# Performance work log

Measured on AMD Instinct MI355X. Metric: run time of the kernel, lower is better.

The kernel has to match this reference:

```python
import jax, jax.numpy as jnp
import numpy as np

T = 8
TAU = 2.0       # spikingjelly LIFNode default tau
VTH = 1.0       # default v_threshold
ALPHA = 2.0     # surrogate.ATan alpha
EPS = 1e-5      # BatchNorm eps


@jax.custom_vjp
def spike_fn(x):
    # Heaviside with ATan surrogate gradient
    return (x >= 0.0).astype(x.dtype)

def _spike_fwd(x):
    return (x >= 0.0).astype(x.dtype), x

def _spike_bwd(x, g):
    sg = (ALPHA / 2.0) / (1.0 + (jnp.pi / 2.0 * ALPHA * x) ** 2)
    return (g * sg,)

spike_fn.defvjp(_spike_fwd, _spike_bwd)


def lif(x_seq):
    """Multi-step LIF over leading time axis. decay_input=True, hard reset to 0, detach_reset."""
    def step(v, x):
        v = v + (x - v) / TAU            # charge
        s = spike_fn(v - VTH)            # fire (surrogate grad)
        v = v * (1.0 - jax.lax.stop_gradient(s))  # detached hard reset to v_reset=0
        return v, s
    _, s_seq = jax.lax.scan(step, jnp.zeros_like(x_seq[0]), x_seq)
    return s_seq


def conv2d(x, w, b, stride):
    y = jax.lax.conv_general_dilated(x, w, (stride, stride), 'VALID',
                                     dimension_numbers=('NCHW', 'OIHW', 'NCHW'))
    return y + b[None, :, None, None]


def batchnorm(x, g, b):
    # training-mode BN over merged (T*B, H, W) axes, matching step_mode='m' BatchNorm2d
    m = x.mean((0, 2, 3), keepdims=True)
    v = x.var((0, 2, 3), keepdims=True)
    return g[None, :, None, None] * (x - m) * jax.lax.rsqrt(v + EPS) + b[None, :, None, None]


def setup_inputs() -> dict:
    key = jax.random.key(0)
    ks = jax.random.split(key, 12)
    def w_init(k, shape):
        fan_in = int(np.prod(shape[1:]))
        return jax.random.normal(k, shape, dtype=jnp.float32) / np.sqrt(fan_in)
    x = jax.random.normal(ks[0], (128, 4, 84, 84), dtype=jnp.float32)
    return {
        'x': x,
        'conv1_w': w_init(ks[1], (32, 4, 8, 8)),  'conv1_b': jnp.zeros((32,), jnp.float32),
        'bn1_g': jnp.ones((32,), jnp.float32),    'bn1_b': jnp.zeros((32,), jnp.float32),
        'conv2_w': w_init(ks[2], (64, 32, 4, 4)), 'conv2_b': jnp.zeros((64,), jnp.float32),
        'bn2_g': jnp.ones((64,), jnp.float32),    'bn2_b': jnp.zeros((64,), jnp.float32),
        'conv3_w': w_init(ks[3], (64, 64, 3, 3)), 'conv3_b': jnp.zeros((64,), jnp.float32),
        'bn3_g': jnp.ones((64,), jnp.float32),    'bn3_b': jnp.zeros((64,), jnp.float32),
        'fc1_w': w_init(ks[4], (512, 3136)),      'fc1_b': jnp.zeros((512,), jnp.float32),
        'fco_w': w_init(ks[5], (2, 512)),         'fco_b': jnp.zeros((2,), jnp.float32),
    }


def reference(x, conv1_w, conv1_b, bn1_g, bn1_b, conv2_w, conv2_b, bn2_g, bn2_b,
              conv3_w, conv3_b, bn3_g, bn3_b, fc1_w, fc1_b, fco_w, fco_b):
    B = x.shape[0]
    # replicate input over T timesteps; fold T into batch for conv/BN (step_mode='m')
    xs = jnp.broadcast_to(x, (T,) + x.shape).reshape((T * B,) + x.shape[1:])

    h = batchnorm(conv2d(xs, conv1_w, conv1_b, 4), bn1_g, bn1_b)   # [TB,32,20,20]
    s = lif(h.reshape((T, B) + h.shape[1:]))
    h = s.reshape((T * B,) + s.shape[2:])

    h = batchnorm(conv2d(h, conv2_w, conv2_b, 2), bn2_g, bn2_b)    # [TB,64,9,9]
    s = lif(h.reshape((T, B) + h.shape[1:]))
    h = s.reshape((T * B,) + s.shape[2:])

    h = batchnorm(conv2d(h, conv3_w, conv3_b, 1), bn3_g, bn3_b)    # [TB,64,7,7]
    s = lif(h.reshape((T, B) + h.shape[1:]))                        # [T,B,64,7,7]

    feat = s.reshape(T, B, -1)                                      # [T,B,3136]
    hid = lif(jnp.einsum('tbi,oi->tbo', feat, fc1_w) + fc1_b)       # [T,B,512]
    out_seq = jnp.einsum('tbo,ko->tbk', hid, fco_w) + fco_b         # [T,B,2]
    return out_seq.mean(0)                                          # [B,2]
```

## Files before the change

### kernel.cpp

```cpp
#include <hip/hip_runtime.h>
#include <cstdint>
#include <cstddef>

#define TT 8

#define H1_ELEMS (128*32*20*20)
#define E2_ELEMS (128*64*81)
#define E3_ELEMS (128*64*49)

typedef __attribute__((ext_vector_type(8))) short short8;
typedef __attribute__((ext_vector_type(4))) float f32x4;

__global__ void prep_wT1(const float* __restrict__ w1, float* __restrict__ wT1) {
  int i = blockIdx.x * 256 + threadIdx.x;
  if (i >= 8192) return;
  int oc = i >> 8, pos = i & 255;
  wT1[(oc >> 4) * 4096 + pos * 16 + (oc & 15)] = w1[oc * 256 + pos];
}

__global__ void prep_w2frag(const float* __restrict__ w2, __bf16* __restrict__ wf) {
  int i = blockIdx.x * 256 + threadIdx.x;
  if (i >= 98304) return;
  int j    = i & 7;
  int oc   = (i >> 3) & 63;
  int quad = (i >> 9) & 3;
  int ksg  = (i >> 11) & 15;
  int term = i >> 15;
  int k = ksg * 32 + quad * 8 + j;
  int ci = k >> 4, kpos = k & 15;
  float w = w2[oc * 512 + ci * 16 + kpos];
  float hf = (float)(__bf16)w;
  float r1 = w - hf;
  float mf = (float)(__bf16)r1;
  float r2 = r1 - mf;
  __bf16 val = (term == 0) ? (__bf16)w : (term == 1) ? (__bf16)r1 : (__bf16)r2;
  wf[i] = val;
}

__global__ void prep_w3frag(const float* __restrict__ w3, __bf16* __restrict__ wf) {
  int i = blockIdx.x * 256 + threadIdx.x;
  if (i >= 110592) return;
  int j    = i & 7;
  int oc   = (i >> 3) & 63;
  int quad = (i >> 9) & 3;
  int tk   = i >> 11;
  int term = tk / 18, kstep = tk % 18;
  int k = kstep * 32 + quad * 8 + j;
  int pos = k >> 6, ci = k & 63;
  float w = w3[oc * 576 + ci * 9 + pos];
  float hf = (float)(__bf16)w;
  float r1 = w - hf;
  float mf = (float)(__bf16)r1;
  float r2 = r1 - mf;
  __bf16 val = (term == 0) ? (__bf16)w : (term == 1) ? (__bf16)r1 : (__bf16)r2;
  wf[i] = val;
}

__global__ void prep_wff(const float* __restrict__ w, __bf16* __restrict__ wf) {
  int i = blockIdx.x * 256 + threadIdx.x;
  if (i >= 602112) return;
  int oc   = i & 511;
  int quad = (i >> 9) & 3;
  int ts   = i >> 11;
  int term = ts / 98, s = ts - term * 98;
  int kbase = s * 32 + quad * 8;
  int pos = kbase >> 6;
  int ci0 = kbase & 63;
  union { __bf16 h[8]; short8 v; } V;
  #pragma unroll
  for (int j = 0; j < 8; j++) {
    float wv = w[(size_t)oc * 3136 + (ci0 + j) * 49 + pos];
    float hf = (float)(__bf16)wv;
    float r1 = wv - hf;
    float mf = (float)(__bf16)r1;
    float r2 = r1 - mf;
    V.h[j] = (term == 0) ? (__bf16)wv : (term == 1) ? (__bf16)r1 : (__bf16)r2;
  }
  *(short8*)(wf + (size_t)i * 8) = V.v;
}

__global__ __launch_bounds__(128) void k_conv1(const float* __restrict__ x,
                                               const float* __restrict__ wT,
                                               const float* __restrict__ bias,
                                               float* __restrict__ out) {
  __shared__ float xt[8064];
  int tid = threadIdx.x;
  int img = blockIdx.x >> 2;
  int q   = blockIdx.x & 3;
  int och = blockIdx.y;
  float4* dst = (float4*)xt;
  #pragma unroll
  for (int ci = 0; ci < 4; ci++) {
    const float4* s4 = (const float4*)(x + (size_t)img * 28224 + ci * 7056 + q * 1680);
    for (int i = tid; i < 504; i += 128) dst[ci * 504 + i] = s4[i];
  }
  __syncthreads();
  if (tid >= 100) return;
  int oyl = tid / 20, ox = tid % 20;
  float acc[16];
  #pragma unroll
  for (int j = 0; j < 16; j++) acc[j] = 0.f;
  int xb0 = oyl * 336 + ox * 4;
  const float* wh = wT + och * 4096;
  #pragma unroll 1
  for (int ci = 0; ci < 4; ci++) {
    #pragma unroll 1
    for (int ky = 0; ky < 8; ky++) {
      const float* xr = xt + ci * 2016 + xb0 + ky * 84;
      float4 xa  = *(const float4*)xr;
      float4 xbv = *(const float4*)(xr + 4);
      const float* wr = wh + (ci * 8 + ky) * 128;
      float xs[8] = {xa.x, xa.y, xa.z, xa.w, xbv.x, xbv.y, xbv.z, xbv.w};
      #pragma unroll
      for (int kx = 0; kx < 8; kx++) {
        #pragma unroll
        for (int j = 0; j < 16; j++)
          acc[j] = fmaf(xs[kx], wr[kx * 16 + j], acc[j]);
      }
    }
  }
  size_t obase = (size_t)img * 12800 + och * 6400 + (q * 5 + oyl) * 20 + ox;
  #pragma unroll
  for (int j = 0; j < 16; j++) out[obase + j * 400] = acc[j] + bias[och * 16 + j];
}

template <int HW>
__global__ void k_bnpartial(const float* __restrict__ xp, int C, int Nper,
                            float* __restrict__ pout) {
  int c = blockIdx.x, s = blockIdx.y, S = gridDim.y, tid = threadIdx.x;
  int n = Nper * HW;
  float sum = 0.f, sum2 = 0.f;
  for (int i = tid; i < n; i += 256) {
    int nb = s * Nper + i / HW;
    int p  = i % HW;
    float v = xp[((size_t)nb * C + c) * HW + p];
    sum += v; sum2 += v * v;
  }
  __shared__ float l0[256], l1[256];
  l0[tid] = sum; l1[tid] = sum2; __syncthreads();
  for (int k = 128; k > 0; k >>= 1) {
    if (tid < k) { l0[tid] += l0[tid + k]; l1[tid] += l1[tid + k]; }
    __syncthreads();
  }
  if (tid == 0) { pout[(c * S + s) * 2] = l0[0]; pout[(c * S + s) * 2 + 1] = l1[0]; }
}

__global__ void k_bnfinal(const float* __restrict__ pin, int S, float n,
                          float* __restrict__ meanArr, float* __restrict__ rstdArr) {
  int c = blockIdx.x, lane = threadIdx.x;
  float s = 0.f, s2 = 0.f;
  if (lane < S) { s = pin[(c * S + lane) * 2]; s2 = pin[(c * S + lane) * 2 + 1]; }
  for (int off = 8; off > 0; off >>= 1) { s += __shfl_down(s, off); s2 += __shfl_down(s2, off); }
  if (lane == 0) {
    float m = s / n;
    float var = s2 / n - m * m;
    meanArr[c] = m;
    rstdArr[c] = rsqrtf(var + 1e-5f);
  }
}

__global__ void k_lif1b(const float* __restrict__ h, const float* __restrict__ mean,
                        const float* __restrict__ rstd, const float* __restrict__ g,
                        const float* __restrict__ bb, uint32_t* __restrict__ sout) {
  int idx = blockIdx.x * 256 + threadIdx.x;
  int ic = idx / 20;
  int ci = ic & 31;
  const float* hp = h + (size_t)idx * 20;
  float gm = g[ci], mm = mean[ci], rs = rstd[ci], bc = bb[ci];
  float xv[20];
  #pragma unroll
  for (int j4 = 0; j4 < 5; j4++) {
    float4 hv = ((const float4*)hp)[j4];
    xv[j4 * 4 + 0] = gm * (hv.x - mm) * rs + bc;
    xv[j4 * 4 + 1] = gm * (hv.y - mm) * rs + bc;
    xv[j4 * 4 + 2] = gm * (hv.z - mm) * rs + bc;
    xv[j4 * 4 + 3] = gm * (hv.w - mm) * rs + bc;
  }
  float v[20];
  #pragma unroll
  for (int j = 0; j < 20; j++) v[j] = 0.f;
  #pragma unroll
  for (int t = 0; t < TT; t++) {
    uint32_t w = 0;
    #pragma unroll
    for (int j = 0; j < 20; j++) {
      v[j] = v[j] + (xv[j] - v[j]) * 0.5f;
      uint32_t s = (v[j] >= 1.0f);
      w |= s << j;
      if (s) v[j] = 0.f;
    }
    sout[t * 81920 + idx] = w;
  }
}

template <int W, int NROW>
__global__ void k_lifb(const float* __restrict__ h, const float* __restrict__ mean,
                       const float* __restrict__ rstd, const float* __restrict__ g,
                       const float* __restrict__ bb, uint32_t* __restrict__ sout,
                       int E) {
  int idx = blockIdx.x * 256 + threadIdx.x;
  int bc = idx / NROW;
  int c = bc & 63;
  float gm = g[c], mm = mean[c], rs = rstd[c], bcn = bb[c];
  float v[W];
  #pragma unroll
  for (int j = 0; j < W; j++) v[j] = 0.f;
  int nword = 128 * 64 * NROW;
  #pragma unroll
  for (int t = 0; t < TT; t++) {
    const float* hp = h + (size_t)t * E + (size_t)idx * W;
    uint32_t w = 0;
    #pragma unroll
    for (int j = 0; j < W; j++) {
      float xv = gm * (hp[j] - mm) * rs + bcn;
      v[j] = v[j] + (xv - v[j]) * 0.5f;
      uint32_t s = (v[j] >= 1.0f);
      w |= s << j;
      if (s) v[j] = 0.f;
    }
    sout[t * nword + idx] = w;
  }
}

__global__ __launch_bounds__(256) void k_conv2m(const uint32_t* __restrict__ s1b,
                                                const __bf16* __restrict__ wf,
                                                const float* __restrict__ bias,
                                                float* __restrict__ out) {
  __shared__ uint32_t sp[1280];
  __shared__ uint4 wl4[3072];
  __bf16* wl = (__bf16*)wl4;
  int tid = threadIdx.x;
  int img0 = blockIdx.x * 2;
  {
    const uint32_t* src = s1b + (size_t)img0 * 640;
    for (int i = tid; i < 1280; i += 256) sp[i] = src[i];
  }
  int wave = tid >> 6, lane = tid & 63;
  int img_local = wave >> 1;
  int tg = wave & 1;
  int l15 = lane & 15, quad = lane >> 4;
  int ci_off = quad >> 1;
  int kyp = (quad & 1) * 2;
  int spb[3], sh[3];
  #pragma unroll
  for (int mt = 0; mt < 3; mt++) {
    int px = tg * 48 + mt * 16 + l15;
    if (px > 80) px = 80;
    int oy = px / 9, ox = px - oy * 9;
    sh[mt]  = ox * 2;
    spb[mt] = img_local * 640 + ci_off * 20 + oy * 2 + kyp;
  }
  f32x4 acc[3][4];
  #pragma unroll
  for (int mt = 0; mt < 3; mt++)
    #pragma unroll
    for (int nt = 0; nt < 4; nt++) acc[mt][nt] = (f32x4){0.f, 0.f, 0.f, 0.f};

  for (int kc = 0; kc < 4; kc++) {
    __syncthreads();
    for (int o = tid * 8; o < 24576; o += 2048) {
      int tk = o >> 11;
      int term = tk >> 2, ksl = tk & 3;
      const __bf16* src = wf + (((term * 16 + kc * 4 + ksl)) << 11) + (o & 2047);
      *(uint4*)(wl + o) = *(const uint4*)src;
    }
    __syncthreads();
    #pragma unroll
    for (int ks = 0; ks < 4; ks++) {
      int ksg = kc * 4 + ks;
      short8 a[3];
      #pragma unroll
      for (int mt = 0; mt < 3; mt++) {
        uint32_t w0 = sp[spb[mt] + ksg * 40];
        uint32_t w1 = sp[spb[mt] + ksg * 40 + 1];
        uint32_t n0 = (w0 >> sh[mt]) & 15u;
        uint32_t n1 = (w1 >> sh[mt]) & 15u;
        union { uint32_t u[4]; short8 v; } A;
        A.u[0] = ((n0 & 1u) ? 0x3F80u : 0u) | ((n0 & 2u) ? 0x3F800000u : 0u);
        A.u[1] = ((n0 & 4u) ? 0x3F80u : 0u) | ((n0 & 8u) ? 0x3F800000u : 0u);
        A.u[2] = ((n1 & 1u) ? 0x3F80u : 0u) | ((n1 & 2u) ? 0x3F800000u : 0u);
        A.u[3] = ((n1 & 4u) ? 0x3F80u : 0u) | ((n1 & 8u) ? 0x3F800000u : 0u);
        a[mt] = A.v;
      }
      #pragma unroll
      for (int term = 0; term < 3; term++) {
        int fb = ((term * 4 + ks) << 11) + (quad << 9);
        #pragma unroll
        for (int nt = 0; nt < 4; nt++) {
          short8 b = *(const short8*)(wl + fb + ((nt << 4) + l15) * 8);
          #pragma unroll
          for (int mt = 0; mt < 3; mt++)
            acc[mt][nt] = __builtin_amdgcn_mfma_f32_16x16x32_bf16(a[mt], b, acc[mt][nt], 0, 0, 0);
        }
      }
    }
  }
  #pragma unroll
  for (int nt = 0; nt < 4; nt++) {
    int oc = nt * 16 + l15;
    float bv = bias[oc];
    float* op = out + ((size_t)(img0 + img_local) * 64 + oc) * 81;
    #pragma unroll
    for (int mt = 0; mt < 3; mt++) {
      int pxr = tg * 48 + mt * 16 + quad * 4;
      #pragma unroll
      for (int r = 0; r < 4; r++) {
        int px = pxr + r;
        if (px < 81) op[px] = acc[mt][nt][r] + bv;
      }
    }
  }
}

__global__ void k_s2T(const uint32_t* __restrict__ sbits, uint32_t* __restrict__ s2T) {
  __shared__ uint32_t sb[576];
  int n = blockIdx.x;
  int t = n >> 7, b = n & 127;
  int tid = threadIdx.x;
  const uint32_t* src = sbits + t * 73728 + b * 576;
  for (int i = tid; i < 576; i += 256) sb[i] = src[i];
  __syncthreads();
  if (tid >= 162) return;
  int half = tid & 1, pc = tid >> 1;
  int r = pc / 9, cpix = pc - r * 9;
  uint32_t w = 0;
  #pragma unroll
  for (int ci = 0; ci < 32; ci++)
    w |= (((sb[(half * 32 + ci) * 9 + r] >> cpix) & 1u) << ci);
  s2T[(size_t)n * 162 + pc * 2 + half] = w;
}

__global__ __launch_bounds__(256) void k_conv3m(const uint32_t* __restrict__ s2T,
                                                const __bf16* __restrict__ wf,
                                                const float* __restrict__ bias,
                                                float* __restrict__ out) {
  __shared__ uint32_t sp[324];
  __shared__ uint4 wl4[4608];
  __bf16* wl = (__bf16*)wl4;
  int tid = threadIdx.x;
  int img0 = blockIdx.x * 2;
  {
    const uint32_t* src = s2T + (size_t)img0 * 162;
    for (int i = tid; i < 324; i += 256) sp[i] = src[i];
  }
  int wave = tid >> 6, lane = tid & 63;
  int img_local = wave >> 1, tg = wave & 1;
  int l15 = lane & 15, quad = lane >> 4;
  int qsh = quad * 8;
  int base[2];
  #pragma unroll
  for (int mt = 0; mt < 2; mt++) {
    int px = tg * 32 + mt * 16 + l15;
    if (px > 48) px = 48;
    int oy = px / 7, ox = px - oy * 7;
    base[mt] = img_local * 162 + (oy * 9 + ox) * 2;
  }
  f32x4 acc[2][4];
  #pragma unroll
  for (int mt = 0; mt < 2; mt++)
    #pragma unroll
    for (int nt = 0; nt < 4; nt++) acc[mt][nt] = (f32x4){0.f, 0.f, 0.f, 0.f};

  #pragma unroll
  for (int kc = 0; kc < 3; kc++) {
    __syncthreads();
    #pragma unroll
    for (int it = 0; it < 18; it++) {
      const __bf16* s = wf + (((it / 6) * 18 + kc * 6 + (it % 6)) << 11) + tid * 8;
      *(uint4*)(wl + (it << 11) + tid * 8) = *(const uint4*)s;
    }
    __syncthreads();
    #pragma unroll
    for (int ksl = 0; ksl < 6; ksl++) {
      int kstep = kc * 6 + ksl;
      int pos = kstep >> 1, cihalf = kstep & 1;
      int ky = pos / 3, kx = pos % 3;
      short8 a[2];
      #pragma unroll
      for (int mt = 0; mt < 2; mt++) {
        uint32_t word = sp[base[mt] + (ky * 9 + kx) * 2 + cihalf];
        uint32_t byt = (word >> qsh) & 255u;
        union { uint32_t u[4]; short8 v; } A;
        A.u[0] = ((byt & 1u)  ? 0x3F80u : 0u) | ((byt & 2u)   ? 0x3F800000u : 0u);
        A.u[1] = ((byt & 4u)  ? 0x3F80u : 0u) | ((byt & 8u)   ? 0x3F800000u : 0u);
        A.u[2] = ((byt & 16u) ? 0x3F80u : 0u) | ((byt & 32u)  ? 0x3F800000u : 0u);
        A.u[3] = ((byt & 64u) ? 0x3F80u : 0u) | ((byt & 128u) ? 0x3F800000u : 0u);
        a[mt] = A.v;
      }
      #pragma unroll
      for (int term = 0; term < 3; term++) {
        int fb = ((term * 6 + ksl) << 11) + (quad << 9);
        #pragma unroll
        for (int nt = 0; nt < 4; nt++) {
          short8 b = *(const short8*)(wl + fb + ((nt << 4) + l15) * 8);
          #pragma unroll
          for (int mt = 0; mt < 2; mt++)
            acc[mt][nt] = __builtin_amdgcn_mfma_f32_16x16x32_bf16(a[mt], b, acc[mt][nt], 0, 0, 0);
        }
      }
    }
  }
  #pragma unroll
  for (int nt = 0; nt < 4; nt++) {
    int oc = nt * 16 + l15;
    float bv = bias[oc];
    float* op = out + ((size_t)(img0 + img_local) * 64 + oc) * 49;
    #pragma unroll
    for (int mt = 0; mt < 2; mt++) {
      int pxr = tg * 32 + mt * 16 + quad * 4;
      #pragma unroll
      for (int r = 0; r < 4; r++) {
        int px = pxr + r;
        if (px < 49) op[px] = acc[mt][nt][r] + bv;
      }
    }
  }
}

__global__ void k_s3T(const uint32_t* __restrict__ sbits, uint32_t* __restrict__ s3T) {
  __shared__ uint32_t sb[896];
  int r0 = blockIdx.x * 2;
  int tid = threadIdx.x;
  for (int i = tid; i < 896; i += 256) {
    int rl = i / 448, o = i - rl * 448;
    int row = r0 + rl;
    sb[i] = sbits[(row >> 7) * 57344 + (row & 127) * 448 + o];
  }
  __syncthreads();
  if (tid >= 196) return;
  int rl = tid / 98, k = tid - rl * 98;
  int pos = k >> 1, half = k & 1;
  int py = pos / 7, px = pos - py * 7;
  const uint32_t* base = sb + rl * 448 + half * 224 + py;
  uint32_t w = 0;
  #pragma unroll
  for (int ci = 0; ci < 32; ci++)
    w |= ((base[ci * 7] >> px) & 1u) << ci;
  s3T[(size_t)(r0 + rl) * 98 + k] = w;
}

__global__ __launch_bounds__(256) void k_fc1m(const uint32_t* __restrict__ s3T,
                                              const __bf16* __restrict__ wf,
                                              float* __restrict__ part) {
  __shared__ uint32_t aS[6272];
  int tid = threadIdx.x;
  int row0 = blockIdx.x * 64;
  int oc0  = blockIdx.y * 32;
  {
    const uint32_t* src = s3T + (size_t)row0 * 98;
    for (int i = tid; i < 6272; i += 256) aS[i] = src[i];
  }
  __syncthreads();
  int wave = tid >> 6, lane = tid & 63;
  int l15 = lane & 15, quad = lane >> 4;
  int qsh = quad * 8;
  f32x4 acc[4][2];
  #pragma unroll
  for (int mt = 0; mt < 4; mt++)
    #pragma unroll
    for (int nt = 0; nt < 2; nt++) acc[mt][nt] = (f32x4){0.f, 0.f, 0.f, 0.f};
  int nIter = (wave < 2) ? 25 : 24;
  #pragma unroll 1
  for (int i = 0; i < nIter; i++) {
    int ks = i * 4 + wave;
    short8 a[4];
    #pragma unroll
    for (int mt = 0; mt < 4; mt++) {
      uint32_t word = aS[(mt * 16 + l15) * 98 + ks];
      uint32_t byt = (word >> qsh) & 255u;
      union { uint32_t u[4]; short8 v; } A;
      A.u[0] = ((byt & 1u)  ? 0x3F80u : 0u) | ((byt & 2u)   ? 0x3F800000u : 0u);
      A.u[1] = ((byt & 4u)  ? 0x3F80u : 0u) | ((byt & 8u)   ? 0x3F800000u : 0u);
      A.u[2] = ((byt & 16u) ? 0x3F80u : 0u) | ((byt & 32u)  ? 0x3F800000u : 0u);
      A.u[3] = ((byt & 64u) ? 0x3F80u : 0u) | ((byt & 128u) ? 0x3F800000u : 0u);
      a[mt] = A.v;
    }
    #pragma unroll
    for (int term = 0; term < 3; term++) {
      size_t fb = ((size_t)((term * 98 + ks) * 4 + quad) * 512 + oc0 + l15) * 8;
      #pragma unroll
      for (int nt = 0; nt < 2; nt++) {
        short8 b = *(const short8*)(wf + fb + nt * 128);
        #pragma unroll
        for (int mt = 0; mt < 4; mt++)
          acc[mt][nt] = __builtin_amdgcn_mfma_f32_16x16x32_bf16(a[mt], b, acc[mt][nt], 0, 0, 0);
      }
    }
  }
  #pragma unroll
  for (int mt = 0; mt < 4; mt++) {
    #pragma unroll
    for (int nt = 0; nt < 2; nt++) {
      int oc = oc0 + nt * 16 + l15;
      #pragma unroll
      for (int r = 0; r < 4; r++) {
        int row = row0 + mt * 16 + quad * 4 + r;
        part[(size_t)wave * 524288 + (size_t)row * 512 + oc] = acc[mt][nt][r];
      }
    }
  }
}

__global__ void k_fc1red_lif(const float* __restrict__ part, const float* __restrict__ bias,
                             unsigned char* __restrict__ hid) {
  int idx = blockIdx.x * 256 + threadIdx.x;
  float bv = bias[idx & 511];
  float v = 0.f;
  #pragma unroll
  for (int t = 0; t < TT; t++) {
    float a = part[t * 65536 + idx];
    #pragma unroll
    for (int j = 1; j < 4; j++) a += part[(size_t)j * 524288 + t * 65536 + idx];
    a += bv;
    v = v + (a - v) * 0.5f;
    unsigned char s = (v >= 1.0f);
    hid[t * 65536 + idx] = s;
    if (s) v = 0.f;
  }
}

__global__ void k_fco(const unsigned char* __restrict__ hid, const float* __restrict__ w,
                      const float* __restrict__ bias, float* __restrict__ out) {
  int b = blockIdx.x, tid = threadIdx.x;
  float a0 = 0.f, a1 = 0.f;
  for (int t = 0; t < TT; t++) {
    const unsigned char* hrow = hid + ((size_t)t * 128 + b) * 512;
    for (int o = tid; o < 512; o += 256) {
      if (hrow[o]) { a0 += w[o]; a1 += w[512 + o]; }
    }
  }
  __shared__ float l0[256], l1[256];
  l0[tid] = a0; l1[tid] = a1; __syncthreads();
  for (int k = 128; k > 0; k >>= 1) {
    if (tid < k) { l0[tid] += l0[tid + k]; l1[tid] += l1[tid + k]; }
    __syncthreads();
  }
  if (tid == 0) {
    out[b * 2 + 0] = l0[0] * 0.125f + bias[0];
    out[b * 2 + 1] = l1[0] * 0.125f + bias[1];
  }
}

extern "C" void kernel_launch(void* const* d_in, const int* in_sizes, int n_in,
                              void* d_out, int out_size, void* d_ws, size_t ws_size,
                              hipStream_t stream) {
  const float* x    = (const float*)d_in[0];
  const float* c1w  = (const float*)d_in[1];
  const float* c1b  = (const float*)d_in[2];
  const float* bn1g = (const float*)d_in[3];
  const float* bn1b = (const float*)d_in[4];
  const float* c2w  = (const float*)d_in[5];
  const float* c2b  = (const float*)d_in[6];
  const float* bn2g = (const float*)d_in[7];
  const float* bn2b = (const float*)d_in[8];
  const float* c3w  = (const float*)d_in[9];
  const float* c3b  = (const float*)d_in[10];
  const float* bn3g = (const float*)d_in[11];
  const float* bn3b = (const float*)d_in[12];
  const float* fc1w = (const float*)d_in[13];
  const float* fc1b = (const float*)d_in[14];
  const float* fcow = (const float*)d_in[15];
  const float* fcob = (const float*)d_in[16];
  float* out = (float*)d_out;

  char* ws = (char*)d_ws;
  float*    h1     = (float*)(ws + 0);
  uint32_t* s1bits = (uint32_t*)(ws + 6553600);
  float*    h2     = (float*)(ws + 19660800);
  uint32_t* s2bits = (uint32_t*)(ws + 40894464);
  float*    h3     = (float*)(ws + 46202880);
  uint32_t* s3bits = (uint32_t*)(ws + 59047936);
  unsigned char* hid = (unsigned char*)(ws + 64356352);
  float*    st     = (float*)(ws + 64880640);
  __bf16*   w2f  = (__bf16*)(ws + 60882944);
  __bf16*   w3f  = (__bf16*)(ws + 61079552);
  uint32_t* s2T  = (uint32_t*)(ws + 61300736);
  float*    wT1  = (float*)(ws + 62390272);
  float*    bnpart = (float*)(ws + 9437184);
  __bf16*   wff    = (__bf16*)(ws + 19660800);
  float*    f1part = (float*)(ws + 29360128);
  uint32_t* s3T    = (uint32_t*)(ws + 43253760);

  prep_wT1   <<<32, 256, 0, stream>>>(c1w, wT1);
  prep_w2frag<<<384, 256, 0, stream>>>(c2w, w2f);
  prep_w3frag<<<432, 256, 0, stream>>>(c3w, w3f);
  k_conv1    <<<dim3(512, 2), 128, 0, stream>>>(x, wT1, c1b, h1);
  k_bnpartial<400><<<dim3(32, 16), 256, 0, stream>>>(h1, 32, 8, bnpart);
  k_bnfinal  <<<32, 64, 0, stream>>>(bnpart, 16, 128.f * 400.f, st, st + 32);
  k_lif1b    <<<320, 256, 0, stream>>>(h1, st, st + 32, bn1g, bn1b, s1bits);

  k_conv2m   <<<512, 256, 0, stream>>>(s1bits, w2f, c2b, h2);
  k_bnpartial<81><<<dim3(64, 16), 256, 0, stream>>>(h2, 64, 64, bnpart);
  k_bnfinal  <<<64, 64, 0, stream>>>(bnpart, 16, 1024.f * 81.f, st + 64, st + 128);
  k_lifb<9, 9><<<288, 256, 0, stream>>>(h2, st + 64, st + 128, bn2g, bn2b, s2bits, E2_ELEMS);
  prep_wff   <<<2352, 256, 0, stream>>>(fc1w, wff);

  k_s2T      <<<1024, 256, 0, stream>>>(s2bits, s2T);
  k_conv3m   <<<512, 256, 0, stream>>>(s2T, w3f, c3b, h3);
  k_bnpartial<49><<<dim3(64, 16), 256, 0, stream>>>(h3, 64, 64, bnpart);
  k_bnfinal  <<<64, 64, 0, stream>>>(bnpart, 16, 1024.f * 49.f, st + 192, st + 256);
  k_lifb<7, 7><<<224, 256, 0, stream>>>(h3, st + 192, st + 256, bn3g, bn3b, s3bits, E3_ELEMS);

  k_s3T      <<<512, 256, 0, stream>>>(s3bits, s3T);
  k_fc1m     <<<dim3(16, 16), 256, 0, stream>>>(s3T, wff, f1part);
  k_fc1red_lif<<<256, 256, 0, stream>>>(f1part, fc1b, hid);
  k_fco      <<<128, 256, 0, stream>>>(hid, fcow, fcob, out);
}
```

Baseline: 288.9 us.

## Fuse BN statistics into conv epilogues, merge weight prep, tile fc1 weight prep

Each conv kernel (conv1, conv2, conv3) now accumulates per-channel sum and sum-of-squares in its epilogue and writes per-block partials. This removes the separate bnpartial passes that re-read h1/h2/h3 from memory, and a new bnfinal2 reduces the 512 partials per channel. The three small weight-prep kernels are merged into one launch. The fc1 weight split is rewritten to stage a tile in shared memory so global reads are coalesced and all three bf16 terms are written at once. The cost is extra syncs and shared-memory reductions in the conv epilogues.

```diff
diff --git a/kernel.cpp b/kernel.cpp
--- a/kernel.cpp
+++ b/kernel.cpp
@@ -4,85 +4,90 @@
 
 #define TT 8
 
-#define H1_ELEMS (128*32*20*20)
 #define E2_ELEMS (128*64*81)
 #define E3_ELEMS (128*64*49)
 
 typedef __attribute__((ext_vector_type(8))) short short8;
 typedef __attribute__((ext_vector_type(4))) float f32x4;
 
-__global__ void prep_wT1(const float* __restrict__ w1, float* __restrict__ wT1) {
+__global__ void prep_all(const float* __restrict__ w1, const float* __restrict__ w2,
+                         const float* __restrict__ w3, float* __restrict__ wT1,
+                         __bf16* __restrict__ w2f, __bf16* __restrict__ w3f) {
   int i = blockIdx.x * 256 + threadIdx.x;
-  if (i >= 8192) return;
-  int oc = i >> 8, pos = i & 255;
-  wT1[(oc >> 4) * 4096 + pos * 16 + (oc & 15)] = w1[oc * 256 + pos];
-}
-
-__global__ void prep_w2frag(const float* __restrict__ w2, __bf16* __restrict__ wf) {
-  int i = blockIdx.x * 256 + threadIdx.x;
-  if (i >= 98304) return;
-  int j    = i & 7;
-  int oc   = (i >> 3) & 63;
-  int quad = (i >> 9) & 3;
-  int ksg  = (i >> 11) & 15;
-  int term = i >> 15;
-  int k = ksg * 32 + quad * 8 + j;
-  int ci = k >> 4, kpos = k & 15;
-  float w = w2[oc * 512 + ci * 16 + kpos];
-  float hf = (float)(__bf16)w;
-  float r1 = w - hf;
-  float mf = (float)(__bf16)r1;
-  float r2 = r1 - mf;
-  __bf16 val = (term == 0) ? (__bf16)w : (term == 1) ? (__bf16)r1 : (__bf16)r2;
-  wf[i] = val;
-}
-
-__global__ void prep_w3frag(const float* __restrict__ w3, __bf16* __restrict__ wf) {
-  int i = blockIdx.x * 256 + threadIdx.x;
-  if (i >= 110592) return;
-  int j    = i & 7;
-  int oc   = (i >> 3) & 63;
-  int quad = (i >> 9) & 3;
-  int tk   = i >> 11;
-  int term = tk / 18, kstep = tk % 18;
-  int k = kstep * 32 + quad * 8 + j;
-  int pos = k >> 6, ci = k & 63;
-  float w = w3[oc * 576 + ci * 9 + pos];
-  float hf = (float)(__bf16)w;
-  float r1 = w - hf;
-  float mf = (float)(__bf16)r1;
-  float r2 = r1 - mf;
-  __bf16 val = (term == 0) ? (__bf16)w : (term == 1) ? (__bf16)r1 : (__bf16)r2;
-  wf[i] = val;
-}
-
-__global__ void prep_wff(const float* __restrict__ w, __bf16* __restrict__ wf) {
-  int i = blockIdx.x * 256 + threadIdx.x;
-  if (i >= 602112) return;
-  int oc   = i & 511;
-  int quad = (i >> 9) & 3;
-  int ts   = i >> 11;
-  int term = ts / 98, s = ts - term * 98;
-  int kbase = s * 32 + quad * 8;
-  int pos = kbase >> 6;
-  int ci0 = kbase & 63;
-  union { __bf16 h[8]; short8 v; } V;
-  #pragma unroll
-  for (int j = 0; j < 8; j++) {
-    float wv = w[(size_t)oc * 3136 + (ci0 + j) * 49 + pos];
-    float hf = (float)(__bf16)wv;
-    float r1 = wv - hf;
+  if (i < 8192) {
+    int oc = i >> 8, pos = i & 255;
+    wT1[(oc >> 4) * 4096 + pos * 16 + (oc & 15)] = w1[oc * 256 + pos];
+  } else if (i < 106496) {
+    int v = i - 8192;
+    int j    = v & 7;
+    int oc   = (v >> 3) & 63;
+    int quad = (v >> 9) & 3;
+    int ksg  = (v >> 11) & 15;
+    int term = v >> 15;
+    int k = ksg * 32 + quad * 8 + j;
+    int ci = k >> 4, kpos = k & 15;
+    float w = w2[oc * 512 + ci * 16 + kpos];
+    float hf = (float)(__bf16)w;
+    float r1 = w - hf;
     float mf = (float)(__bf16)r1;
     float r2 = r1 - mf;
-    V.h[j] = (term == 0) ? (__bf16)wv : (term == 1) ? (__bf16)r1 : (__bf16)r2;
-  }
-  *(short8*)(wf + (size_t)i * 8) = V.v;
+    w2f[v] = (term == 0) ? (__bf16)w : (term == 1) ? (__bf16)r1 : (__bf16)r2;
+  } else if (i < 217088) {
+    int v = i - 106496;
+    int j    = v & 7;
+    int oc   = (v >> 3) & 63;
+    int quad = (v >> 9) & 3;
+    int tk   = v >> 11;
+    int term = tk / 18, kstep = tk % 18;
+    int k = kstep * 32 + quad * 8 + j;
+    int pos = k >> 6, ci = k & 63;
+    float w = w3[oc * 576 + ci * 9 + pos];
+    float hf = (float)(__bf16)w;
+    float r1 = w - hf;
+    float mf = (float)(__bf16)r1;
+    float r2 = r1 - mf;
+    w3f[v] = (term == 0) ? (__bf16)w : (term == 1) ? (__bf16)r1 : (__bf16)r2;
+  }
+}
+
+__global__ __launch_bounds__(256) void prep_wff(const float* __restrict__ w,
+                                                __bf16* __restrict__ wf) {
+  __shared__ float tile[12544];
+  int oc0 = blockIdx.x * 32;
+  int ci0 = blockIdx.y * 8;
+  int tid = threadIdx.x;
+  for (int f = tid; f < 12544; f += 256) {
+    int oc_l = f / 392, r = f - oc_l * 392;
+    tile[f] = w[(size_t)(oc0 + oc_l) * 3136 + ci0 * 49 + r];
+  }
+  __syncthreads();
+  int squad = (ci0 & 31) >> 3;
+  int sadd  = ci0 >> 5;
+  for (int g = tid; g < 1568; g += 256) {
+    int pos = g >> 5, oc_l = g & 31;
+    union { __bf16 h[8]; uint4 u; } T0, T1, T2;
+    #pragma unroll
+    for (int j = 0; j < 8; j++) {
+      float wv = tile[oc_l * 392 + j * 49 + pos];
+      float hf = (float)(__bf16)wv;
+      float r1 = wv - hf;
+      float mf = (float)(__bf16)r1;
+      float r2 = r1 - mf;
+      T0.h[j] = (__bf16)wv; T1.h[j] = (__bf16)r1; T2.h[j] = (__bf16)r2;
+    }
+    int s = pos * 2 + sadd;
+    size_t b0 = (((size_t)s * 4 + squad) * 512 + oc0 + oc_l) * 8;
+    *(uint4*)(wf + b0)               = T0.u;
+    *(uint4*)(wf + b0 + 1605632)     = T1.u;
+    *(uint4*)(wf + b0 + 3211264)     = T2.u;
+  }
 }
 
 __global__ __launch_bounds__(128) void k_conv1(const float* __restrict__ x,
                                                const float* __restrict__ wT,
                                                const float* __restrict__ bias,
-                                               float* __restrict__ out) {
+                                               float* __restrict__ out,
+                                               float* __restrict__ pout) {
   __shared__ float xt[8064];
   int tid = threadIdx.x;
   int img = blockIdx.x >> 2;
@@ -95,65 +100,75 @@
     for (int i = tid; i < 504; i += 128) dst[ci * 504 + i] = s4[i];
   }
   __syncthreads();
-  if (tid >= 100) return;
+  bool active = tid < 100;
   int oyl = tid / 20, ox = tid % 20;
   float acc[16];
   #pragma unroll
   for (int j = 0; j < 16; j++) acc[j] = 0.f;
-  int xb0 = oyl * 336 + ox * 4;
-  const float* wh = wT + och * 4096;
-  #pragma unroll 1
-  for (int ci = 0; ci < 4; ci++) {
+  if (active) {
+    int xb0 = oyl * 336 + ox * 4;
+    const float* wh = wT + och * 4096;
     #pragma unroll 1
-    for (int ky = 0; ky < 8; ky++) {
-      const float* xr = xt + ci * 2016 + xb0 + ky * 84;
-      float4 xa  = *(const float4*)xr;
-      float4 xbv = *(const float4*)(xr + 4);
-      const float* wr = wh + (ci * 8 + ky) * 128;
-      float xs[8] = {xa.x, xa.y, xa.z, xa.w, xbv.x, xbv.y, xbv.z, xbv.w};
-      #pragma unroll
-      for (int kx = 0; kx < 8; kx++) {
+    for (int ci = 0; ci < 4; ci++) {
+      #pragma unroll 1
+      for (int ky = 0; ky < 8; ky++) {
+        const float* xr = xt + ci * 2016 + xb0 + ky * 84;
+        float4 xa  = *(const float4*)xr;
+        float4 xbv = *(const float4*)(xr + 4);
+        const float* wr = wh + (ci * 8 + ky) * 128;
+        float xs[8] = {xa.x, xa.y, xa.z, xa.w, xbv.x, xbv.y, xbv.z, xbv.w};
         #pragma unroll
-        for (int j = 0; j < 16; j++)
-          acc[j] = fmaf(xs[kx], wr[kx * 16 + j], acc[j]);
-      }
-    }
-  }
+        for (int kx = 0; kx < 8; kx++) {
+          #pragma unroll
+          for (int j = 0; j < 16; j++)
+            acc[j] = fmaf(xs[kx], wr[kx * 16 + j], acc[j]);
+        }
+      }
+    }
+  }
+  __syncthreads();
   size_t obase = (size_t)img * 12800 + och * 6400 + (q * 5 + oyl) * 20 + ox;
   #pragma unroll
-  for (int j = 0; j < 16; j++) out[obase + j * 400] = acc[j] + bias[och * 16 + j];
-}
-
-template <int HW>
-__global__ void k_bnpartial(const float* __restrict__ xp, int C, int Nper,
-                            float* __restrict__ pout) {
-  int c = blockIdx.x, s = blockIdx.y, S = gridDim.y, tid = threadIdx.x;
-  int n = Nper * HW;
-  float sum = 0.f, sum2 = 0.f;
-  for (int i = tid; i < n; i += 256) {
-    int nb = s * Nper + i / HW;
-    int p  = i % HW;
-    float v = xp[((size_t)nb * C + c) * HW + p];
-    sum += v; sum2 += v * v;
-  }
+  for (int j = 0; j < 16; j++) {
+    float v = 0.f;
+    if (active) {
+      v = acc[j] + bias[och * 16 + j];
+      out[obase + j * 400] = v;
+    }
+    xt[j * 128 + tid] = v;
+    xt[2048 + j * 128 + tid] = v * v;
+  }
+  __syncthreads();
+  for (int off = 64; off > 0; off >>= 1) {
+    if (tid < off) {
+      #pragma unroll
+      for (int j = 0; j < 16; j++) {
+        xt[j * 128 + tid] += xt[j * 128 + tid + off];
+        xt[2048 + j * 128 + tid] += xt[2048 + j * 128 + tid + off];
+      }
+    }
+    __syncthreads();
+  }
+  if (tid < 16) {
+    pout[(och * 16 + tid) * 512 + blockIdx.x] = xt[tid * 128];
+    pout[16384 + (och * 16 + tid) * 512 + blockIdx.x] = xt[2048 + tid * 128];
+  }
+}
+
+__global__ void k_bnfinal2(const float* __restrict__ pin, int sqoff, float n,
+                           float* __restrict__ meanArr, float* __restrict__ rstdArr) {
   __shared__ float l0[256], l1[256];
-  l0[tid] = sum; l1[tid] = sum2; __syncthreads();
+  int c = blockIdx.x, tid = threadIdx.x;
+  l0[tid] = pin[c * 512 + tid] + pin[c * 512 + tid + 256];
+  l1[tid] = pin[sqoff + c * 512 + tid] + pin[sqoff + c * 512 + tid + 256];
+  __syncthreads();
   for (int k = 128; k > 0; k >>= 1) {
     if (tid < k) { l0[tid] += l0[tid + k]; l1[tid] += l1[tid + k]; }
     __syncthreads();
   }
-  if (tid == 0) { pout[(c * S + s) * 2] = l0[0]; pout[(c * S + s) * 2 + 1] = l1[0]; }
-}
-
-__global__ void k_bnfinal(const float* __restrict__ pin, int S, float n,
-                          float* __restrict__ meanArr, float* __restrict__ rstdArr) {
-  int c = blockIdx.x, lane = threadIdx.x;
-  float s = 0.f, s2 = 0.f;
-  if (lane < S) { s = pin[(c * S + lane) * 2]; s2 = pin[(c * S + lane) * 2 + 1]; }
-  for (int off = 8; off > 0; off >>= 1) { s += __shfl_down(s, off); s2 += __shfl_down(s2, off); }
-  if (lane == 0) {
-    float m = s / n;
-    float var = s2 / n - m * m;
+  if (tid == 0) {
+    float m = l0[0] / n;
+    float var = l1[0] / n - m * m;
     meanArr[c] = m;
     rstdArr[c] = rsqrtf(var + 1e-5f);
   }
@@ -225,7 +240,8 @@
 __global__ __launch_bounds__(256) void k_conv2m(const uint32_t* __restrict__ s1b,
                                                 const __bf16* __restrict__ wf,
                                                 const float* __restrict__ bias,
-                                                float* __restrict__ out) {
+                                                float* __restrict__ out,
+                                                float* __restrict__ pout) {
   __shared__ uint32_t sp[1280];
   __shared__ uint4 wl4[3072];
   __bf16* wl = (__bf16*)wl4;
@@ -295,8 +311,10 @@
       }
     }
   }
+  float sl[4], sl2[4];
   #pragma unroll
   for (int nt = 0; nt < 4; nt++) {
+    sl[nt] = 0.f; sl2[nt] = 0.f;
     int oc = nt * 16 + l15;
     float bv = bias[oc];
     float* op = out + ((size_t)(img0 + img_local) * 64 + oc) * 81;
@@ -306,9 +324,29 @@
       #pragma unroll
       for (int r = 0; r < 4; r++) {
         int px = pxr + r;
-        if (px < 81) op[px] = acc[mt][nt][r] + bv;
-      }
-    }
+        if (px < 81) {
+          float v = acc[mt][nt][r] + bv;
+          op[px] = v;
+          sl[nt] += v; sl2[nt] += v * v;
+        }
+      }
+    }
+  }
+  __syncthreads();
+  float* sred = (float*)wl4;
+  #pragma unroll
+  for (int nt = 0; nt < 4; nt++) {
+    int idx = (nt * 16 + l15) * 16 + (wave * 4 + quad);
+    sred[idx] = sl[nt];
+    sred[1024 + idx] = sl2[nt];
+  }
+  __syncthreads();
+  if (tid < 64) {
+    float s = 0.f, s2 = 0.f;
+    #pragma unroll
+    for (int k = 0; k < 16; k++) { s += sred[tid * 16 + k]; s2 += sred[1024 + tid * 16 + k]; }
+    pout[tid * 512 + blockIdx.x] = s;
+    pout[32768 + tid * 512 + blockIdx.x] = s2;
   }
 }
 
@@ -333,7 +371,8 @@
 __global__ __launch_bounds__(256) void k_conv3m(const uint32_t* __restrict__ s2T,
                                                 const __bf16* __restrict__ wf,
                                                 const float* __restrict__ bias,
-                                                float* __restrict__ out) {
+                                                float* __restrict__ out,
+                                                float* __restrict__ pout) {
   __shared__ uint32_t sp[324];
   __shared__ uint4 wl4[4608];
   __bf16* wl = (__bf16*)wl4;
@@ -400,8 +439,10 @@
       }
     }
   }
+  float sl[4], sl2[4];
   #pragma unroll
   for (int nt = 0; nt < 4; nt++) {
+    sl[nt] = 0.f; sl2[nt] = 0.f;
     int oc = nt * 16 + l15;
     float bv = bias[oc];
     float* op = out + ((size_t)(img0 + img_local) * 64 + oc) * 49;
@@ -411,9 +452,29 @@
       #pragma unroll
       for (int r = 0; r < 4; r++) {
         int px = pxr + r;
-        if (px < 49) op[px] = acc[mt][nt][r] + bv;
-      }
-    }
+        if (px < 49) {
+          float v = acc[mt][nt][r] + bv;
+          op[px] = v;
+          sl[nt] += v; sl2[nt] += v * v;
+        }
+      }
+    }
+  }
+  __syncthreads();
+  float* sred = (float*)wl4;
+  #pragma unroll
+  for (int nt = 0; nt < 4; nt++) {
+    int idx = (nt * 16 + l15) * 16 + (wave * 4 + quad);
+    sred[idx] = sl[nt];
+    sred[1024 + idx] = sl2[nt];
+  }
+  __syncthreads();
+  if (tid < 64) {
+    float s = 0.f, s2 = 0.f;
+    #pragma unroll
+    for (int k = 0; k < 16; k++) { s += sred[tid * 16 + k]; s2 += sred[1024 + tid * 16 + k]; }
+    pout[tid * 512 + blockIdx.x] = s;
+    pout[32768 + tid * 512 + blockIdx.x] = s2;
   }
 }
 
@@ -581,24 +642,19 @@
   float*    f1part = (float*)(ws + 29360128);
   uint32_t* s3T    = (uint32_t*)(ws + 43253760);
 
-  prep_wT1   <<<32, 256, 0, stream>>>(c1w, wT1);
-  prep_w2frag<<<384, 256, 0, stream>>>(c2w, w2f);
-  prep_w3frag<<<432, 256, 0, stream>>>(c3w, w3f);
-  k_conv1    <<<dim3(512, 2), 128, 0, stream>>>(x, wT1, c1b, h1);
-  k_bnpartial<400><<<dim3(32, 16), 256, 0, stream>>>(h1, 32, 8, bnpart);
-  k_bnfinal  <<<32, 64, 0, stream>>>(bnpart, 16, 128.f * 400.f, st, st + 32);
+  prep_all   <<<848, 256, 0, stream>>>(c1w, c2w, c3w, wT1, w2f, w3f);
+  k_conv1    <<<dim3(512, 2), 128, 0, stream>>>(x, wT1, c1b, h1, bnpart);
+  k_bnfinal2 <<<32, 256, 0, stream>>>(bnpart, 16384, 51200.f, st, st + 32);
   k_lif1b    <<<320, 256, 0, stream>>>(h1, st, st + 32, bn1g, bn1b, s1bits);
 
-  k_conv2m   <<<512, 256, 0, stream>>>(s1bits, w2f, c2b, h2);
-  k_bnpartial<81><<<dim3(64, 16), 256, 0, stream>>>(h2, 64, 64, bnpart);
-  k_bnfinal  <<<64, 64, 0, stream>>>(bnpart, 16, 1024.f * 81.f, st + 64, st + 128);
+  k_conv2m   <<<512, 256, 0, stream>>>(s1bits, w2f, c2b, h2, bnpart);
+  k_bnfinal2 <<<64, 256, 0, stream>>>(bnpart, 32768, 82944.f, st + 64, st + 128);
   k_lifb<9, 9><<<288, 256, 0, stream>>>(h2, st + 64, st + 128, bn2g, bn2b, s2bits, E2_ELEMS);
-  prep_wff   <<<2352, 256, 0, stream>>>(fc1w, wff);
+  prep_wff   <<<dim3(16, 8), 256, 0, stream>>>(fc1w, wff);
 
   k_s2T      <<<1024, 256, 0, stream>>>(s2bits, s2T);
-  k_conv3m   <<<512, 256, 0, stream>>>(s2T, w3f, c3b, h3);
-  k_bnpartial<49><<<dim3(64, 16), 256, 0, stream>>>(h3, 64, 64, bnpart);
-  k_bnfinal  <<<64, 64, 0, stream>>>(bnpart, 16, 1024.f * 49.f, st + 192, st + 256);
+  k_conv3m   <<<512, 256, 0, stream>>>(s2T, w3f, c3b, h3, bnpart);
+  k_bnfinal2 <<<64, 256, 0, stream>>>(bnpart, 32768, 50176.f, st + 192, st + 256);
   k_lifb<7, 7><<<224, 256, 0, stream>>>(h3, st + 192, st + 256, bn3g, bn3b, s3bits, E3_ELEMS);
 
   k_s3T      <<<512, 256, 0, stream>>>(s3bits, s3T);
```

Result: faster. 260.8 us (-9.7%).
